# Kernel optimization log

Hardware: AMD Instinct MI355X
Metric: run time of the kernel (lower is better)

The kernel has to match this reference:

```python
import jax, jax.numpy as jnp
import numpy as np

B, S, W = 64, 512, 16
E, TE, CE, CC = 300, 50, 50, 50
HID, TGT = 256, 16
VOCAB, TAGV, CHARV = 5002, 50, 100
IN = E + TE + CC  # 400


def setup_inputs() -> dict:
    key = jax.random.key(0)
    ks = jax.random.split(key, 24)
    sc = 0.1
    embed_table = (jax.random.normal(ks[0], (VOCAB, E)) * sc).at[0].set(0.0)
    tag_table = (jax.random.normal(ks[1], (TAGV, TE)) * sc).at[0].set(0.0)
    char_table = (jax.random.normal(ks[2], (CHARV, CE)) * sc).at[0].set(0.0)
    return {
        "X": jax.random.randint(ks[3], (B, S), 0, VOCAB),
        "labels_m": jax.random.uniform(ks[4], (B, S)),
        "tags": jax.random.randint(ks[5], (B, S), 0, TAGV),
        "chars": jax.random.randint(ks[6], (B, S, W), 0, CHARV),
        "embed_table": embed_table,
        "tag_table": tag_table,
        "char_table": char_table,
        "conv_w": jax.random.normal(ks[7], (CC, CE, 3)) * sc,
        "conv_b": jax.random.normal(ks[8], (CC,)) * sc,
        "w_ih_f": jax.random.normal(ks[9], (4 * HID, IN)) * sc,
        "w_hh_f": jax.random.normal(ks[10], (4 * HID, HID)) * sc,
        "b_ih_f": jax.random.normal(ks[11], (4 * HID,)) * sc,
        "b_hh_f": jax.random.normal(ks[12], (4 * HID,)) * sc,
        "w_ih_b": jax.random.normal(ks[13], (4 * HID, IN)) * sc,
        "w_hh_b": jax.random.normal(ks[14], (4 * HID, HID)) * sc,
        "b_ih_b": jax.random.normal(ks[15], (4 * HID,)) * sc,
        "b_hh_b": jax.random.normal(ks[16], (4 * HID,)) * sc,
        "fc_w": jax.random.normal(ks[17], (TGT, 2 * HID)) * sc,
        "fc_b": jax.random.normal(ks[18], (TGT,)) * sc,
        "A": jax.random.normal(ks[19], (TGT, TGT)),
        "wd": jax.random.normal(ks[20], (2 * HID,)),
    }


def _lstm_dir(xs, w_ih, w_hh, b_ih, b_hh, reverse):
    # xs: [S, B, IN] ; PyTorch gate order i,f,g,o
    h0 = jnp.zeros((xs.shape[1], w_hh.shape[1]), xs.dtype)

    def step(carry, x):
        h, c = carry
        g = x @ w_ih.T + h @ w_hh.T + (b_ih + b_hh)
        i, f, gg, o = jnp.split(g, 4, axis=-1)
        c = jax.nn.sigmoid(f) * c + jax.nn.sigmoid(i) * jnp.tanh(gg)
        h = jax.nn.sigmoid(o) * jnp.tanh(c)
        return (h, c), h

    _, hs = jax.lax.scan(step, (h0, h0), xs, reverse=reverse)
    return hs


def _features(X, labels_m, tags, chars, embed_table, tag_table, char_table,
              conv_w, conv_b, w_ih_f, w_hh_f, b_ih_f, b_hh_f,
              w_ih_b, w_hh_b, b_ih_b, b_hh_b, fc_w, fc_b, wd):
    embed = embed_table[X]          # [B,S,E]
    tag_embed = tag_table[tags]     # [B,S,TE]
    ce = char_table[chars]          # [B,S,W,CE]
    ce = ce.transpose(0, 3, 1, 2).reshape(B, CE, S * W)  # [B,CE,S*W]
    conv = jax.lax.conv_general_dilated(
        ce, conv_w, window_strides=(1,), padding=((1, 1),),
        dimension_numbers=("NCH", "OIH", "NCH")) + conv_b[None, :, None]
    char_conv = conv.reshape(B, CC, S, W).max(axis=3).transpose(0, 2, 1)  # [B,S,CC]
    feat = jnp.concatenate([embed, tag_embed, char_conv], axis=2)  # [B,S,IN]
    xs = feat.transpose(1, 0, 2)  # [S,B,IN]
    hf = _lstm_dir(xs, w_ih_f, w_hh_f, b_ih_f, b_hh_f, reverse=False)
    hb = _lstm_dir(xs, w_ih_b, w_hh_b, b_ih_b, b_hh_b, reverse=True)
    H = jnp.concatenate([hf, hb], axis=-1).transpose(1, 0, 2)  # [B,S,2H]
    H = H + labels_m[:, :, None] * wd[None, None, :]
    return H @ fc_w.T + fc_b  # [B,S,TGT]


def _viterbi(P, A):
    Xs = P.transpose(1, 0, 2)  # [S,B,T]
    b_idx = jnp.arange(P.shape[0])

    def vstep(delta, x):
        scores = delta[:, :, None] + A[None] + x[:, None, :]  # [B,prev,cur]
        return scores.max(axis=1), (scores.max(axis=1), scores.argmax(axis=1))

    deltaL, (drest, psis) = jax.lax.scan(vstep, Xs[0], Xs[1:])
    deltas = jnp.concatenate([Xs[0][None], drest], axis=0)  # [S,B,T]
    psi_end = deltaL.argmax(axis=1)                          # [B]
    score0 = deltaL[b_idx, psi_end]

    def back(carry, inp):
        tag, sc = carry
        psi_t, delta_t = inp
        prev = psi_t[b_idx, tag]
        return (prev, sc + delta_t[b_idx, prev]), prev

    (_, score), prevs = jax.lax.scan(back, (psi_end, score0),
                                     (psis, deltas[:-1]), reverse=True)
    path = jnp.concatenate([prevs, psi_end[None]], axis=0).T  # [B,S]
    return path, score


def reference(X, labels_m, tags, chars, embed_table, tag_table, char_table,
              conv_w, conv_b, w_ih_f, w_hh_f, b_ih_f, b_hh_f,
              w_ih_b, w_hh_b, b_ih_b, b_hh_b, fc_w, fc_b, A, wd):
    P = _features(X, labels_m, tags, chars, embed_table, tag_table, char_table,
                  conv_w, conv_b, w_ih_f, w_hh_f, b_ih_f, b_hh_f,
                  w_ih_b, w_hh_b, b_ih_b, b_hh_b, fc_w, fc_b, wd)
    return _viterbi(P, A)
```

## Files before the change

kernel.cpp:

```cpp
#include <hip/hip_runtime.h>


#define DEV __device__ __forceinline__
typedef unsigned short u16;
typedef unsigned int   u32;
typedef unsigned char  u8;
typedef signed char    s8;
using short8  = __attribute__((ext_vector_type(8))) short;
using f32x4   = __attribute__((ext_vector_type(4))) float;
using int4v   = __attribute__((ext_vector_type(4))) int;

DEV float bf2f(u16 u){ union{u32 i; float f;} v; v.i = ((u32)u)<<16; return v.f; }
DEV u16 f2bf(float f){ u32 x = __float_as_uint(f); return (u16)((x + 0x7fffu + ((x>>16)&1u)) >> 16); }
DEV u32 pk2(float a, float b){ return (u32)f2bf(a) | ((u32)f2bf(b) << 16); }
DEV float sigf(float x){ return __builtin_amdgcn_rcpf(1.f + __expf(-x)); }
DEV float tanh_f(float x){ return 1.f - 2.f*__builtin_amdgcn_rcpf(__expf(2.f*x) + 1.f); }
DEV float rdlane_f(float v, int l){
  return __uint_as_float(__builtin_amdgcn_readlane(__float_as_uint(v), l));
}

typedef __attribute__((address_space(1))) const u32 GU;
typedef __attribute__((address_space(3))) u32 LU;
DEV void gld_lds16(const void* g, void* l){
  __builtin_amdgcn_global_load_lds((GU*)g, (LU*)l, 16, 0, 0);
}
DEV void bar_l(){
  __builtin_amdgcn_sched_barrier(0);
  asm volatile("s_waitcnt lgkmcnt(0)" ::: "memory");
  __builtin_amdgcn_s_barrier();
  __builtin_amdgcn_sched_barrier(0);
}

static const size_t OFF_GI   = 0;
static const size_t OFF_P    = 0;
static const size_t OFF_DL   = OFF_P  + (size_t)32768*16*4;
static const size_t OFF_PSI  = OFF_DL + (size_t)32768*16*4;
static const size_t OFF_B    = (size_t)134217728;
static const size_t OFF_WIH  = OFF_B    + (size_t)33554432;
static const size_t OFF_WQ   = OFF_WIH  + (size_t)1703936;
static const size_t OFF_SC   = OFF_WQ   + (size_t)524288;
static const size_t OFF_BIAS = OFF_SC   + 8192;
static const size_t OFF_WFC  = OFF_BIAS + 8192;
static const size_t REQUIRED = OFF_WFC  + 256;

__global__ __launch_bounds__(256) void k01_fused(
    const int* __restrict__ X, const int* __restrict__ tg, const int* __restrict__ ch,
    const float* __restrict__ etab, const float* __restrict__ ttab, const float* __restrict__ ctab,
    const float* __restrict__ cw, const float* __restrict__ cb, u16* __restrict__ feat,
    const float* __restrict__ whhf, const float* __restrict__ whhb,
    s8* __restrict__ wq, float* __restrict__ sc2,
    const float* bihf, const float* bhhf, const float* bihb, const float* bhhb,
    const float* fcw, const float* wdp, float* bias, float* wfc,
    const float* __restrict__ wihf, const float* __restrict__ wihb, u16* __restrict__ wih)
{
  __shared__ float smem[3960 + 7800];
  const int tid = threadIdx.x;
  const int bid = blockIdx.x;

  if (bid < 1024){
    float* ce_s = smem;
    float* w_s  = smem + 3960;
    const int b = bid >> 4, sbb = bid & 15;
    for (int i = tid; i < 7500; i += 256){
      int cc = i/150, r2 = i - cc*150;
      int ce = r2/3, dc = r2 - ce*3;
      w_s[(cc*3 + dc)*52 + ce] = cw[i];
    }
    const int li = tid & 15, jg = tid >> 4;
    float stg[13];

    #define GATHER(T) { \
      const int sbg = sbb*8 + (T); \
      _Pragma("unroll") \
      for (int j = 0; j < 13; j++){ \
        int i = tid + 256*j; \
        float v = 0.f; \
        if (i < 3300){ \
          int qq = i/50, ce = i - qq*50; \
          int p = sbg*64 - 1 + qq; \
          if (p >= 0 && p < 8192){ int ci = ch[b*8192 + p]; v = ctab[ci*50 + ce]; } \
        } \
        stg[j] = v; \
      } }

    GATHER(0);
    for (int t = 0; t < 8; t++){
      const int sb = sbb*8 + t;
      bar_l();
      #pragma unroll
      for (int j = 0; j < 13; j++){
        int i = tid + 256*j;
        if (i < 3300){
          int qq = i/50, ce = i - qq*50;
          ce_s[qq*60 + ce] = stg[j];
        }
      }
      bar_l();
      if (t < 7) GATHER(t+1);

      float acc[4][3];
      #pragma unroll
      for (int k=0;k<4;k++){ acc[k][0]=0.f; acc[k][1]=0.f; acc[k][2]=0.f; }
      #pragma unroll
      for (int dc = 0; dc < 3; dc++){
        for (int ceb = 0; ceb < 48; ceb += 4){
          f32x4 w0 = *(const f32x4*)&w_s[((3*jg+0)*3 + dc)*52 + ceb];
          f32x4 w1 = *(const f32x4*)&w_s[((3*jg+1)*3 + dc)*52 + ceb];
          f32x4 w2 = *(const f32x4*)&w_s[((3*jg+2)*3 + dc)*52 + ceb];
          #pragma unroll
          for (int k = 0; k < 4; k++){
            f32x4 cv = *(const f32x4*)&ce_s[(16*k + li + dc)*60 + ceb];
            #pragma unroll
            for (int e = 0; e < 4; e++){
              acc[k][0] += cv[e]*w0[e];
              acc[k][1] += cv[e]*w1[e];
              acc[k][2] += cv[e]*w2[e];
            }
          }
        }
        float w0a = w_s[((3*jg+0)*3+dc)*52 + 48], w0b = w_s[((3*jg+0)*3+dc)*52 + 49];
        float w1a = w_s[((3*jg+1)*3+dc)*52 + 48], w1b = w_s[((3*jg+1)*3+dc)*52 + 49];
        float w2a = w_s[((3*jg+2)*3+dc)*52 + 48], w2b = w_s[((3*jg+2)*3+dc)*52 + 49];
        #pragma unroll
        for (int k = 0; k < 4; k++){
          float ca  = ce_s[(16*k + li + dc)*60 + 48];
          float cb2 = ce_s[(16*k + li + dc)*60 + 49];
          acc[k][0] += ca*w0a + cb2*w0b;
          acc[k][1] += ca*w1a + cb2*w1b;
          acc[k][2] += ca*w2a + cb2*w2b;
        }
      }
      #pragma unroll
      for (int m = 1; m < 16; m <<= 1)
        #pragma unroll
        for (int k=0;k<4;k++)
          #pragma unroll
          for (int c=0;c<3;c++)
            acc[k][c] = fmaxf(acc[k][c], __shfl_xor(acc[k][c], m, 64));
      if (li == 0){
        #pragma unroll
        for (int k=0;k<4;k++)
          #pragma unroll
          for (int c=0;c<3;c++){
            int cc = 3*jg + c;
            int s = sb*4 + k;
            feat[(size_t)(s*64 + b)*416 + 350 + cc] = f2bf(acc[k][c] + cb[cc]);
          }
      }
      if (tid < 128){
        int pl = tid & 63, cc = 48 + (tid >> 6);
        float a2 = 0.f;
        #pragma unroll
        for (int dc = 0; dc < 3; dc++){
          for (int ceb = 0; ceb < 48; ceb += 4){
            f32x4 wv = *(const f32x4*)&w_s[(cc*3 + dc)*52 + ceb];
            f32x4 cv = *(const f32x4*)&ce_s[(pl + dc)*60 + ceb];
            a2 += cv[0]*wv[0] + cv[1]*wv[1] + cv[2]*wv[2] + cv[3]*wv[3];
          }
          a2 += ce_s[(pl+dc)*60 + 48]*w_s[(cc*3+dc)*52 + 48]
              + ce_s[(pl+dc)*60 + 49]*w_s[(cc*3+dc)*52 + 49];
        }
        #pragma unroll
        for (int m = 1; m < 16; m <<= 1) a2 = fmaxf(a2, __shfl_xor(a2, m, 64));
        if ((tid & 15) == 0){
          int s = sb*4 + ((tid & 63) >> 4);
          feat[(size_t)(s*64 + b)*416 + 350 + cc] = f2bf(a2 + cb[cc]);
        }
      }
    }
    #undef GATHER
    return;
  }

  if (bid < 3072){
    const int cid = bid - 1024;
    const int w = tid >> 6, lane = tid & 63;
    #pragma unroll
    for (int r = 0; r < 4; r++){
      const int m = cid*16 + w*4 + r;
      const int s = m >> 6, b = m & 63;
      const int xi = X[b*512 + s];
      const int ti = tg[b*512 + s];
      u32* dst = (u32*)feat + (size_t)m*208;
      #pragma unroll
      for (int pass = 0; pass < 3; pass++){
        int word = pass*64 + lane;
        if (word < 150){
          float2 f = *(const float2*)(etab + (size_t)xi*300 + word*2);
          dst[word] = pk2(f.x, f.y);
        } else if (word < 175){
          float2 f = *(const float2*)(ttab + (size_t)ti*50 + (word-150)*2);
          dst[word] = pk2(f.x, f.y);
        } else if (word < 183){
          dst[200 + word - 175] = 0u;
        }
      }
    }
    return;
  }

  const int bx = bid - 3072;
  if (bx > 512){
    const int n = bx - 513;
    const float* src = (n < 1024) ? (wihf + (size_t)n*400) : (wihb + (size_t)(n-1024)*400);
    u32* dst = (u32*)(wih + (size_t)n*416);
    if (tid < 208){
      int j = tid*2;
      u32 v = 0u;
      if (j < 400){
        float2 f = *(const float2*)(src + j);
        v = pk2(f.x, f.y);
      }
      dst[tid] = v;
    }
    return;
  }
  if (bx == 512){
    float* red = smem;
    for (int n = tid; n < 2048; n += 256){
      bias[n] = (n < 1024) ? (bihf[n] + bhhf[n]) : (bihb[n-1024] + bhhb[n-1024]);
    }
    const int cur = tid & 15, part = tid >> 4;
    float s = 0.f;
    for (int k = part*32; k < part*32 + 32; k++) s += fcw[cur*512 + k] * wdp[k];
    red[tid] = s;
    __syncthreads();
    if (tid < 16){
      float t = 0.f;
      #pragma unroll
      for (int p = 0; p < 16; p++) t += red[p*16 + tid];
      wfc[tid] = t;
    }
    return;
  }
  {
    const int row = bx*4 + (tid >> 6);
    const int lane = tid & 63;
    const float* src = (row < 1024) ? (whhf + (size_t)row*256)
                                    : (whhb + (size_t)(row-1024)*256);
    f32x4 v = *(const f32x4*)(src + lane*4);
    float m = fmaxf(fmaxf(fabsf(v[0]), fabsf(v[1])), fmaxf(fabsf(v[2]), fabsf(v[3])));
    #pragma unroll
    for (int d = 1; d < 64; d <<= 1) m = fmaxf(m, __shfl_xor(m, d, 64));
    float inv = 127.f / (m + 1e-30f);
    u32 pack = 0;
    #pragma unroll
    for (int e = 0; e < 4; e++){
      int q = (int)rintf(v[e]*inv);
      q = q > 127 ? 127 : (q < -127 ? -127 : q);
      pack |= ((u32)(u8)(s8)q) << (8*e);
    }
    const int dir = row >> 10, n = row & 1023;
    const int g = n >> 8, j = n & 255, w2 = j >> 4, lr2 = j & 15;
    const int kk = lane >> 4, lq2 = (lane >> 2) & 3, e4 = lane & 3;
    u32* wq32 = (u32*)wq;
    wq32[dir*65536 + (((g*16 + w2)*4 + kk)*64 + lq2*16 + lr2)*4 + e4] = pack;
    if (lane == 0) sc2[row] = m * (1.f/16129.f);
  }
}

__global__ __launch_bounds__(256) void k2_gemm(
    const u16* __restrict__ featp, const u16* __restrict__ wihp,
    const float* __restrict__ bias, u16* __restrict__ gi)
{
  const int m0 = blockIdx.y*128, n0 = blockIdx.x*128;
  const int tid = threadIdx.x, wv = tid>>6, lane = tid&63;
  const int lr = lane & 15, lq = lane >> 4;
  const int wm = (wv>>1)*64, wn = (wv&1)*64;
  __shared__ u16 As[2][4096], Bs[2][4096];
  f32x4 acc[4][4];
  #pragma unroll
  for (int a=0;a<4;a++)
    #pragma unroll
    for (int c=0;c<4;c++) acc[a][c] = (f32x4){0.f,0.f,0.f,0.f};

  #define K2_STAGE(BUF, K0) { \
    _Pragma("unroll") \
    for (int i = 0; i < 2; i++){ \
      int c = i*4 + wv; \
      gld_lds16(featp + (size_t)(m0 + c*16 + (lane>>2))*416 + (K0) + (lane&3)*8, &As[BUF][c*512]); \
      gld_lds16(wihp  + (size_t)(n0 + c*16 + (lane>>2))*416 + (K0) + (lane&3)*8, &Bs[BUF][c*512]); \
    } }

  K2_STAGE(0, 0);
  __syncthreads();
  int buf = 0;
  for (int ki = 0; ki < 13; ki++){
    if (ki < 12) K2_STAGE(buf^1, (ki+1)*32);
    short8 af[4], bfr[4];
    #pragma unroll
    for (int mt=0; mt<4; mt++) af[mt]  = *(const short8*)(&As[buf][0] + (wm + mt*16 + lr)*32 + lq*8);
    #pragma unroll
    for (int nt=0; nt<4; nt++) bfr[nt] = *(const short8*)(&Bs[buf][0] + (wn + nt*16 + lr)*32 + lq*8);
    #pragma unroll
    for (int mt=0; mt<4; mt++)
      #pragma unroll
      for (int nt=0; nt<4; nt++)
        acc[mt][nt] = __builtin_amdgcn_mfma_f32_16x16x32_bf16(af[mt], bfr[nt], acc[mt][nt], 0,0,0);
    __syncthreads();
    buf ^= 1;
  }
  #undef K2_STAGE
  #pragma unroll
  for (int nt=0; nt<4; nt++){
    float bv = bias[n0 + wn + nt*16 + lr];
    #pragma unroll
    for (int mt=0; mt<4; mt++)
      #pragma unroll
      for (int r=0; r<4; r++)
        gi[(size_t)(m0 + wm + mt*16 + lq*4 + r)*2048 + n0 + wn + nt*16 + lr]
            = f2bf(acc[mt][nt][r] + bv);
  }
}

__global__ __launch_bounds__(512, 2) void k3_lstm(
    const s8* __restrict__ wq, const float* __restrict__ sc2,
    const u16* __restrict__ gi, u16* __restrict__ hcat)
{
  const int dir = blockIdx.x >> 5;
  const int bb  = (blockIdx.x & 31) * 2;
  const int tid = threadIdx.x;
  const int w = tid >> 6, lane = tid & 63;
  const int lr = lane & 15, lq = lane >> 4;
  const int cb = tid >> 8, cj = tid & 255;

  __shared__ s8 Hs[2][4096];
  __shared__ float xbuf[2048];

  const s8* wqd = wq + dir*262144;
  int4v bq[2][4][4];
  #pragma unroll
  for (int sl = 0; sl < 2; sl++)
    #pragma unroll
    for (int g = 0; g < 4; g++)
      #pragma unroll
      for (int kk = 0; kk < 4; kk++)
        bq[sl][g][kk] = *(const int4v*)(wqd + (((((g*16 + 2*w + sl)*4 + kk)*64) + lane) << 4));

  float scl[4];
  #pragma unroll
  for (int g = 0; g < 4; g++) scl[g] = sc2[dir*1024 + g*256 + cj];

  *(uint2*)&Hs[0][tid*8] = (uint2){0u,0u};
  *(uint2*)&Hs[1][tid*8] = (uint2){0u,0u};

  float cst = 0.f;
  const ptrdiff_t dstep = dir ? -(ptrdiff_t)131072 : (ptrdiff_t)131072;
  const u16* g0 = gi + (size_t)((dir ? 511 : 0)*64 + bb + cb)*2048 + dir*1024 + cj;
  u32 gcur[4], gn1[4], gn2[4];
  #pragma unroll
  for (int g = 0; g < 4; g++) gcur[g] = g0[g*256];
  const u16* g1 = g0 + dstep;
  #pragma unroll
  for (int g = 0; g < 4; g++) gn1[g] = g1[g*256];
  const u16* gpref = g1;
  __syncthreads();

  #pragma unroll 1
  for (int t = 0; t < 512; t++){
    const int s = dir ? (511 - t) : t;
    if (t + 2 < 512) gpref += dstep;
    #pragma unroll
    for (int g = 0; g < 4; g++) gn2[g] = gpref[g*256];
    const s8* hb = Hs[t & 1];
    int4v aq[4];
    #pragma unroll
    for (int kk = 0; kk < 4; kk++)
      aq[kk] = *(const int4v*)(hb + lr*256 + ((kk*64 + lq*16) ^ (lr << 4)));
    int4v acc[2][4];
    #pragma unroll
    for (int sl = 0; sl < 2; sl++)
      #pragma unroll
      for (int g = 0; g < 4; g++) acc[sl][g] = (int4v){0,0,0,0};
    __builtin_amdgcn_s_setprio(1);
    #pragma unroll
    for (int kk = 0; kk < 4; kk++)
      #pragma unroll
      for (int sl = 0; sl < 2; sl++)
        #pragma unroll
        for (int g = 0; g < 4; g++)
          acc[sl][g] = __builtin_amdgcn_mfma_i32_16x16x64_i8(aq[kk], bq[sl][g][kk], acc[sl][g], 0,0,0);
    __builtin_amdgcn_s_setprio(0);
    if (lq == 0){
      #pragma unroll
      for (int sl = 0; sl < 2; sl++){
        const int j = (2*w + sl)*16 + lr;
        #pragma unroll
        for (int r = 0; r < 2; r++){
          f32x4 v = (f32x4){(float)acc[sl][0][r], (float)acc[sl][1][r],
                            (float)acc[sl][2][r], (float)acc[sl][3][r]};
          *(f32x4*)&xbuf[(r*256 + j)*4] = v;
        }
      }
    }
    bar_l();
    f32x4 p = *(const f32x4*)&xbuf[tid*4];
    float g4[4];
    #pragma unroll
    for (int g = 0; g < 4; g++) g4[g] = bf2f((u16)gcur[g]) + p[g]*scl[g];
    float iv = sigf(g4[0]), fv = sigf(g4[1]);
    float gg = tanh_f(g4[2]), ov = sigf(g4[3]);
    float c = fv*cst + iv*gg;
    cst = c;
    float h = ov * tanh_f(c);
    hcat[(size_t)(s*64 + bb + cb)*512 + dir*256 + cj] = f2bf(h);
    Hs[(t + 1) & 1][cb*256 + (cj ^ (cb << 4))] = (s8)(int)rintf(h * 127.f);
    #pragma unroll
    for (int g = 0; g < 4; g++){ gcur[g] = gn1[g]; gn1[g] = gn2[g]; }
    bar_l();
  }
}

__global__ __launch_bounds__(256) void k4_fc(
    const u16* __restrict__ hcat, const float* __restrict__ fcw, const float* __restrict__ fcb,
    const float* __restrict__ lmp, const float* __restrict__ wfc, float* __restrict__ Pout)
{
  const int wv = threadIdx.x >> 6, lane = threadIdx.x & 63;
  const int lr = lane & 15, lq = lane >> 4;
  const int mt = blockIdx.x*4 + wv;
  short8 bfr[16];
  #pragma unroll
  for (int kk = 0; kk < 16; kk++){
    const float* wr = fcw + (size_t)lr*512 + kk*32 + lq*8;
    f32x4 w0 = *(const f32x4*)wr;
    f32x4 w1 = *(const f32x4*)(wr + 4);
    short8 sv;
    #pragma unroll
    for (int e = 0; e < 4; e++){ sv[e] = (short)f2bf(w0[e]); sv[4+e] = (short)f2bf(w1[e]); }
    bfr[kk] = sv;
  }
  f32x4 acc = (f32x4){0.f,0.f,0.f,0.f};
  #pragma unroll
  for (int kk = 0; kk < 16; kk++){
    short8 af = *(const short8*)(hcat + (size_t)(mt*16 + lr)*512 + kk*32 + lq*8);
    acc = __builtin_amdgcn_mfma_f32_16x16x32_bf16(af, bfr[kk], acc, 0,0,0);
  }
  const int cur = lr;
  float fb = fcb[cur];
  float wf = wfc[cur];
  #pragma unroll
  for (int r = 0; r < 4; r++){
    int m = mt*16 + lq*4 + r;
    int b = m & 63, s = m >> 6;
    float lmv = lmp[b*512 + s];
    Pout[(size_t)m*16 + cur] = acc[r] + fb + lmv*wf;
  }
}

__global__ __launch_bounds__(64) void k5_vit(
    const float* __restrict__ Pg, const float* __restrict__ Am,
    float* __restrict__ dout, float* __restrict__ dl, u8* __restrict__ psi)
{
  const int b = blockIdx.x, lane = threadIdx.x;
  const int cur = lane & 15;
  float Ar[16];
  #pragma unroll
  for (int p = 0; p < 16; p++) Ar[p] = Am[p*16 + cur];
  float dreg[16];
  {
    float v0 = Pg[(size_t)b*16 + cur];
    if (lane < 16) dl[(size_t)b*16 + cur] = v0;
    #pragma unroll
    for (int c = 0; c < 16; c++) dreg[c] = rdlane_f(v0, c);
  }

#define FSTEP(X, S) { \
    float v_[16]; \
    _Pragma("unroll") \
    for (int p = 0; p < 16; p++) v_[p] = dreg[p] + Ar[p]; \
    float m1[8]; int i1[8]; \
    _Pragma("unroll") \
    for (int k = 0; k < 8; k++){ bool c_ = v_[2*k] >= v_[2*k+1]; \
      m1[k] = c_ ? v_[2*k] : v_[2*k+1]; i1[k] = c_ ? 2*k : 2*k+1; } \
    float m2[4]; int i2[4]; \
    _Pragma("unroll") \
    for (int k = 0; k < 4; k++){ bool c_ = m1[2*k] >= m1[2*k+1]; \
      m2[k] = c_ ? m1[2*k] : m1[2*k+1]; i2[k] = c_ ? i1[2*k] : i1[2*k+1]; } \
    float m3[2]; int i3[2]; \
    _Pragma("unroll") \
    for (int k = 0; k < 2; k++){ bool c_ = m2[2*k] >= m2[2*k+1]; \
      m3[k] = c_ ? m2[2*k] : m2[2*k+1]; i3[k] = c_ ? i2[2*k] : i2[2*k+1]; } \
    bool cf_ = m3[0] >= m3[1]; \
    float best = (cf_ ? m3[0] : m3[1]) + (X); \
    int bi = cf_ ? i3[0] : i3[1]; \
    if (lane < 16){ \
      dl[(size_t)((S)*64 + b)*16 + cur] = best; \
      psi[(size_t)((S)*64 + b)*16 + cur] = (u8)bi; \
    } \
    _Pragma("unroll") \
    for (int c = 0; c < 16; c++) dreg[c] = rdlane_f(best, c); \
  }

  float x0 = Pg[(size_t)(1*64 + b)*16 + cur];
  float x1 = Pg[(size_t)(2*64 + b)*16 + cur];
  float x2 = Pg[(size_t)(3*64 + b)*16 + cur];
  float x3 = Pg[(size_t)(4*64 + b)*16 + cur];
  for (int s = 1; s < 512; s += 4){
    FSTEP(x0, s);
    if (s + 4 < 512) x0 = Pg[(size_t)((s+4)*64 + b)*16 + cur];
    if (s + 1 < 512) FSTEP(x1, s+1);
    if (s + 5 < 512) x1 = Pg[(size_t)((s+5)*64 + b)*16 + cur];
    if (s + 2 < 512) FSTEP(x2, s+2);
    if (s + 6 < 512) x2 = Pg[(size_t)((s+6)*64 + b)*16 + cur];
    if (s + 3 < 512) FSTEP(x3, s+3);
    if (s + 7 < 512) x3 = Pg[(size_t)((s+7)*64 + b)*16 + cur];
  }
#undef FSTEP

  float bv = dreg[0]; int bix = 0;
  #pragma unroll
  for (int c = 1; c < 16; c++){ if (dreg[c] > bv){ bv = dreg[c]; bix = c; } }
  int tag = bix;
  float score = bv;
  if (lane == 0) dout[b*512 + 511] = (float)tag;

#define BSTEP(PV, DV, T) { \
    int prev = __builtin_amdgcn_readlane((PV), tag); \
    score += rdlane_f((DV), prev); \
    if (lane == 0) dout[b*512 + (T)] = (float)prev; \
    tag = prev; }

  int   p0 = 0, p1 = 0, p2 = 0, p3 = 0;
  float d0 = 0.f, d1 = 0.f, d2 = 0.f, d3 = 0.f;
  if (lane < 16){
    p0 = psi[(size_t)(511*64 + b)*16 + lane]; d0 = dl[(size_t)(510*64 + b)*16 + lane];
    p1 = psi[(size_t)(510*64 + b)*16 + lane]; d1 = dl[(size_t)(509*64 + b)*16 + lane];
    p2 = psi[(size_t)(509*64 + b)*16 + lane]; d2 = dl[(size_t)(508*64 + b)*16 + lane];
    p3 = psi[(size_t)(508*64 + b)*16 + lane]; d3 = dl[(size_t)(507*64 + b)*16 + lane];
  }
  for (int t = 510; t >= 0; t -= 4){
    BSTEP(p0, d0, t);
    if (t - 4 >= 0 && lane < 16){
      p0 = psi[(size_t)((t-3)*64 + b)*16 + lane]; d0 = dl[(size_t)((t-4)*64 + b)*16 + lane];
    }
    if (t - 1 >= 0) BSTEP(p1, d1, t-1);
    if (t - 5 >= 0 && lane < 16){
      p1 = psi[(size_t)((t-4)*64 + b)*16 + lane]; d1 = dl[(size_t)((t-5)*64 + b)*16 + lane];
    }
    if (t - 2 >= 0) BSTEP(p2, d2, t-2);
    if (t - 6 >= 0 && lane < 16){
      p2 = psi[(size_t)((t-5)*64 + b)*16 + lane]; d2 = dl[(size_t)((t-6)*64 + b)*16 + lane];
    }
    if (t - 3 >= 0) BSTEP(p3, d3, t-3);
    if (t - 7 >= 0 && lane < 16){
      p3 = psi[(size_t)((t-6)*64 + b)*16 + lane]; d3 = dl[(size_t)((t-7)*64 + b)*16 + lane];
    }
  }
#undef BSTEP
  if (lane == 0) dout[32768 + b] = score;
}

extern "C" void kernel_launch(void* const* d_in, const int* in_sizes, int n_in,
                              void* d_out, int out_size, void* d_ws, size_t ws_size,
                              hipStream_t stream)
{
  (void)in_sizes; (void)n_in; (void)out_size;
  if (ws_size < REQUIRED) return;

  const int*   X    = (const int*)d_in[0];
  const float* lm   = (const float*)d_in[1];
  const int*   tg   = (const int*)d_in[2];
  const int*   ch   = (const int*)d_in[3];
  const float* etab = (const float*)d_in[4];
  const float* ttab = (const float*)d_in[5];
  const float* ctab = (const float*)d_in[6];
  const float* cw   = (const float*)d_in[7];
  const float* cb   = (const float*)d_in[8];
  const float* wihf = (const float*)d_in[9];
  const float* whhf = (const float*)d_in[10];
  const float* bihf = (const float*)d_in[11];
  const float* bhhf = (const float*)d_in[12];
  const float* wihb = (const float*)d_in[13];
  const float* whhb = (const float*)d_in[14];
  const float* bihb = (const float*)d_in[15];
  const float* bhhb = (const float*)d_in[16];
  const float* fcw  = (const float*)d_in[17];
  const float* fcb  = (const float*)d_in[18];
  const float* Am   = (const float*)d_in[19];
  const float* wdp  = (const float*)d_in[20];

  char* ws = (char*)d_ws;
  u16*   gi   = (u16*)(ws + OFF_GI);
  u16*   feat = (u16*)(ws + OFF_B);
  u16*   hcat = (u16*)(ws + OFF_B);
  u16*   wih  = (u16*)(ws + OFF_WIH);
  s8*    wq   = (s8*)(ws + OFF_WQ);
  float* sc2  = (float*)(ws + OFF_SC);
  float* Pg   = (float*)(ws + OFF_P);
  float* dlt  = (float*)(ws + OFF_DL);
  u8*    psi  = (u8*)(ws + OFF_PSI);
  float* bias = (float*)(ws + OFF_BIAS);
  float* wfc  = (float*)(ws + OFF_WFC);
  float* dout = (float*)d_out;

  k01_fused<<<5633, 256, 0, stream>>>(X, tg, ch, etab, ttab, ctab, cw, cb, feat,
                                      whhf, whhb, wq, sc2,
                                      bihf, bhhf, bihb, bhhb, fcw, wdp, bias, wfc,
                                      wihf, wihb, wih);
  k2_gemm<<<dim3(16, 256), 256, 0, stream>>>(feat, wih, bias, gi);
  k3_lstm<<<64, 512, 0, stream>>>(wq, sc2, gi, hcat);
  k4_fc<<<512, 256, 0, stream>>>(hcat, fcw, fcb, lm, wfc, Pg);
  k5_vit<<<64, 64, 0, stream>>>(Pg, Am, dout, dlt, psi);
}
```

Before: 1.072 ms.

## Compute char CNN with bf16 MFMA on swizzled LDS tiles

The character convolution in the fused prologue kernel moves from scalar fp32 FMAs over per-timestep staging loops to bf16 MFMA 16x16x32 matrix ops. Each block now covers 256 character positions, with the character embeddings and conv weights staged once into XOR-swizzled LDS, and the max over word positions is reduced through MFMA output lanes. Blocks for this stage go from 1024 to 2048 and all later block index offsets shift to match. Inputs are rounded to bf16 and the K dimension is padded to 192, which costs some precision and wastes part of the MFMA work.

```diff
diff --git a/kernel.cpp b/kernel.cpp
--- a/kernel.cpp
+++ b/kernel.cpp
@@ -43,6 +43,9 @@
 static const size_t OFF_WFC  = OFF_BIAS + 8192;
 static const size_t REQUIRED = OFF_WFC  + 256;
 
+#define CEB(r, byo) ((r)*128 + ((byo) ^ (((r)&7)<<4)))
+#define WBB(r, byo) (33024 + (r)*384 + ((byo) ^ (((r)&7)<<4)))
+
 __global__ __launch_bounds__(256) void k01_fused(
     const int* __restrict__ X, const int* __restrict__ tg, const int* __restrict__ ch,
     const float* __restrict__ etab, const float* __restrict__ ttab, const float* __restrict__ ctab,
@@ -53,127 +56,83 @@
     const float* fcw, const float* wdp, float* bias, float* wfc,
     const float* __restrict__ wihf, const float* __restrict__ wihb, u16* __restrict__ wih)
 {
-  __shared__ float smem[3960 + 7800];
+  __shared__ float smemf[14400];
+  char* sm = (char*)smemf;
   const int tid = threadIdx.x;
   const int bid = blockIdx.x;
 
-  if (bid < 1024){
-    float* ce_s = smem;
-    float* w_s  = smem + 3960;
-    const int b = bid >> 4, sbb = bid & 15;
-    for (int i = tid; i < 7500; i += 256){
-      int cc = i/150, r2 = i - cc*150;
-      int ce = r2/3, dc = r2 - ce*3;
-      w_s[(cc*3 + dc)*52 + ce] = cw[i];
-    }
-    const int li = tid & 15, jg = tid >> 4;
-    float stg[13];
-
-    #define GATHER(T) { \
-      const int sbg = sbb*8 + (T); \
-      _Pragma("unroll") \
-      for (int j = 0; j < 13; j++){ \
-        int i = tid + 256*j; \
-        float v = 0.f; \
-        if (i < 3300){ \
-          int qq = i/50, ce = i - qq*50; \
-          int p = sbg*64 - 1 + qq; \
-          if (p >= 0 && p < 8192){ int ci = ch[b*8192 + p]; v = ctab[ci*50 + ce]; } \
-        } \
-        stg[j] = v; \
-      } }
-
-    GATHER(0);
-    for (int t = 0; t < 8; t++){
-      const int sb = sbb*8 + t;
-      bar_l();
-      #pragma unroll
-      for (int j = 0; j < 13; j++){
-        int i = tid + 256*j;
-        if (i < 3300){
-          int qq = i/50, ce = i - qq*50;
-          ce_s[qq*60 + ce] = stg[j];
-        }
-      }
-      bar_l();
-      if (t < 7) GATHER(t+1);
-
-      float acc[4][3];
-      #pragma unroll
-      for (int k=0;k<4;k++){ acc[k][0]=0.f; acc[k][1]=0.f; acc[k][2]=0.f; }
-      #pragma unroll
-      for (int dc = 0; dc < 3; dc++){
-        for (int ceb = 0; ceb < 48; ceb += 4){
-          f32x4 w0 = *(const f32x4*)&w_s[((3*jg+0)*3 + dc)*52 + ceb];
-          f32x4 w1 = *(const f32x4*)&w_s[((3*jg+1)*3 + dc)*52 + ceb];
-          f32x4 w2 = *(const f32x4*)&w_s[((3*jg+2)*3 + dc)*52 + ceb];
-          #pragma unroll
-          for (int k = 0; k < 4; k++){
-            f32x4 cv = *(const f32x4*)&ce_s[(16*k + li + dc)*60 + ceb];
-            #pragma unroll
-            for (int e = 0; e < 4; e++){
-              acc[k][0] += cv[e]*w0[e];
-              acc[k][1] += cv[e]*w1[e];
-              acc[k][2] += cv[e]*w2[e];
-            }
-          }
-        }
-        float w0a = w_s[((3*jg+0)*3+dc)*52 + 48], w0b = w_s[((3*jg+0)*3+dc)*52 + 49];
-        float w1a = w_s[((3*jg+1)*3+dc)*52 + 48], w1b = w_s[((3*jg+1)*3+dc)*52 + 49];
-        float w2a = w_s[((3*jg+2)*3+dc)*52 + 48], w2b = w_s[((3*jg+2)*3+dc)*52 + 49];
+  if (bid < 2048){
+    const int b = bid >> 5, sg = bid & 31;
+    for (int i = tid; i < 6144; i += 256){
+      int row = i/96, pair = i - row*96;
+      int k0 = pair*2;
+      int dc = k0 >> 6, ce = k0 & 63;
+      float v0 = 0.f, v1 = 0.f;
+      if (row < 50 && ce < 50){
+        v0 = cw[row*150 + ce*3 + dc];
+        if (ce + 1 < 50) v1 = cw[row*150 + (ce+1)*3 + dc];
+      }
+      *(u32*)(sm + WBB(row, pair*4)) = pk2(v0, v1);
+    }
+    for (int i = tid; i < 8256; i += 256){
+      int row = i >> 5, pair = i & 31;
+      int ce0 = pair*2;
+      float v0 = 0.f, v1 = 0.f;
+      int pl = sg*256 - 1 + row;
+      if (pl >= 0 && pl < 8192 && ce0 < 50){
+        int ci = ch[b*8192 + pl];
+        float2 f = *(const float2*)(ctab + (size_t)ci*50 + ce0);
+        v0 = f.x; v1 = f.y;
+      }
+      *(u32*)(sm + CEB(row, pair*4)) = pk2(v0, v1);
+    }
+    __syncthreads();
+
+    const int wv = tid >> 6, lane = tid & 63;
+    const int lr = lane & 15, lq = lane >> 4;
+    f32x4 acc[4][4];
+    #pragma unroll
+    for (int mt = 0; mt < 4; mt++)
+      #pragma unroll
+      for (int nt = 0; nt < 4; nt++) acc[mt][nt] = (f32x4){0.f,0.f,0.f,0.f};
+    #pragma unroll
+    for (int kk = 0; kk < 6; kk++){
+      const int kp = kk*32 + lq*8;
+      const int dc = kp >> 6, ce8 = kp & 63;
+      short8 bfr[4], af[4];
+      #pragma unroll
+      for (int nt = 0; nt < 4; nt++)
+        bfr[nt] = *(const short8*)(sm + WBB(nt*16 + lr, kp*2));
+      #pragma unroll
+      for (int mt = 0; mt < 4; mt++){
+        const int pos = (wv*4 + mt)*16 + lr;
+        af[mt] = *(const short8*)(sm + CEB(pos + dc, ce8*2));
+      }
+      #pragma unroll
+      for (int mt = 0; mt < 4; mt++)
         #pragma unroll
-        for (int k = 0; k < 4; k++){
-          float ca  = ce_s[(16*k + li + dc)*60 + 48];
-          float cb2 = ce_s[(16*k + li + dc)*60 + 49];
-          acc[k][0] += ca*w0a + cb2*w0b;
-          acc[k][1] += ca*w1a + cb2*w1b;
-          acc[k][2] += ca*w2a + cb2*w2b;
-        }
-      }
-      #pragma unroll
-      for (int m = 1; m < 16; m <<= 1)
-        #pragma unroll
-        for (int k=0;k<4;k++)
-          #pragma unroll
-          for (int c=0;c<3;c++)
-            acc[k][c] = fmaxf(acc[k][c], __shfl_xor(acc[k][c], m, 64));
-      if (li == 0){
-        #pragma unroll
-        for (int k=0;k<4;k++)
-          #pragma unroll
-          for (int c=0;c<3;c++){
-            int cc = 3*jg + c;
-            int s = sb*4 + k;
-            feat[(size_t)(s*64 + b)*416 + 350 + cc] = f2bf(acc[k][c] + cb[cc]);
-          }
-      }
-      if (tid < 128){
-        int pl = tid & 63, cc = 48 + (tid >> 6);
-        float a2 = 0.f;
-        #pragma unroll
-        for (int dc = 0; dc < 3; dc++){
-          for (int ceb = 0; ceb < 48; ceb += 4){
-            f32x4 wv = *(const f32x4*)&w_s[(cc*3 + dc)*52 + ceb];
-            f32x4 cv = *(const f32x4*)&ce_s[(pl + dc)*60 + ceb];
-            a2 += cv[0]*wv[0] + cv[1]*wv[1] + cv[2]*wv[2] + cv[3]*wv[3];
-          }
-          a2 += ce_s[(pl+dc)*60 + 48]*w_s[(cc*3+dc)*52 + 48]
-              + ce_s[(pl+dc)*60 + 49]*w_s[(cc*3+dc)*52 + 49];
-        }
-        #pragma unroll
-        for (int m = 1; m < 16; m <<= 1) a2 = fmaxf(a2, __shfl_xor(a2, m, 64));
-        if ((tid & 15) == 0){
-          int s = sb*4 + ((tid & 63) >> 4);
-          feat[(size_t)(s*64 + b)*416 + 350 + cc] = f2bf(a2 + cb[cc]);
-        }
-      }
-    }
-    #undef GATHER
+        for (int nt = 0; nt < 4; nt++)
+          acc[mt][nt] = __builtin_amdgcn_mfma_f32_16x16x32_bf16(af[mt], bfr[nt], acc[mt][nt], 0,0,0);
+    }
+    #pragma unroll
+    for (int mt = 0; mt < 4; mt++){
+      const int s = sg*16 + wv*4 + mt;
+      #pragma unroll
+      for (int nt = 0; nt < 4; nt++){
+        float m = fmaxf(fmaxf(acc[mt][nt][0], acc[mt][nt][1]),
+                        fmaxf(acc[mt][nt][2], acc[mt][nt][3]));
+        m = fmaxf(m, __shfl_xor(m, 16, 64));
+        m = fmaxf(m, __shfl_xor(m, 32, 64));
+        const int cc = nt*16 + lr;
+        if (lq == 0 && cc < 50)
+          feat[(size_t)(s*64 + b)*416 + 350 + cc] = f2bf(m + cb[cc]);
+      }
+    }
     return;
   }
 
-  if (bid < 3072){
-    const int cid = bid - 1024;
+  if (bid < 4096){
+    const int cid = bid - 2048;
     const int w = tid >> 6, lane = tid & 63;
     #pragma unroll
     for (int r = 0; r < 4; r++){
@@ -199,7 +158,7 @@
     return;
   }
 
-  const int bx = bid - 3072;
+  const int bx = bid - 4096;
   if (bx > 512){
     const int n = bx - 513;
     const float* src = (n < 1024) ? (wihf + (size_t)n*400) : (wihb + (size_t)(n-1024)*400);
@@ -216,7 +175,7 @@
     return;
   }
   if (bx == 512){
-    float* red = smem;
+    float* red = smemf;
     for (int n = tid; n < 2048; n += 256){
       bias[n] = (n < 1024) ? (bihf[n] + bhhf[n]) : (bihb[n-1024] + bhhb[n-1024]);
     }
@@ -258,6 +217,8 @@
     if (lane == 0) sc2[row] = m * (1.f/16129.f);
   }
 }
+#undef CEB
+#undef WBB
 
 __global__ __launch_bounds__(256) void k2_gemm(
     const u16* __restrict__ featp, const u16* __restrict__ wihp,
@@ -593,7 +554,7 @@
   float* wfc  = (float*)(ws + OFF_WFC);
   float* dout = (float*)d_out;
 
-  k01_fused<<<5633, 256, 0, stream>>>(X, tg, ch, etab, ttab, ctab, cw, cb, feat,
+  k01_fused<<<6657, 256, 0, stream>>>(X, tg, ch, etab, ttab, ctab, cw, cb, feat,
                                       whhf, whhb, wq, sc2,
                                       bihf, bhhf, bihb, bhhb, fcw, wdp, bias, wfc,
                                       wihf, wihb, wih);
```

Result: faster. 963.7 us (-10.1%).
